# Kernel optimization log

Hardware: AMD Instinct MI355X
Metric: run time of the kernel (lower is better)

The kernel has to match this reference:

```python
import jax, jax.numpy as jnp
import numpy as np

N_NODES = 50000
N_EDGES = 800000
D = 64
STEPS = 10
NEG_SLOPE = 0.2


def setup_inputs() -> dict:
    key = jax.random.key(0)
    ks = jax.random.split(key, 9)
    x = jax.random.normal(ks[0], (N_NODES, D), dtype=jnp.float32)
    edge_index_l1 = jax.random.randint(ks[1], (2, N_EDGES), 0, N_NODES, dtype=jnp.int64 if jax.config.jax_enable_x64 else jnp.int32)
    edge_index_l2 = jax.random.randint(ks[2], (2, N_EDGES), 0, N_NODES, dtype=jnp.int64 if jax.config.jax_enable_x64 else jnp.int32)
    s = 1.0 / np.sqrt(D)
    W1 = jax.random.normal(ks[3], (D, D), dtype=jnp.float32) * s
    a1_src = jax.random.normal(ks[4], (D,), dtype=jnp.float32) * s
    a1_dst = jax.random.normal(ks[5], (D,), dtype=jnp.float32) * s
    W2 = jax.random.normal(ks[6], (D, D), dtype=jnp.float32) * s
    a2_src = jax.random.normal(ks[7], (D,), dtype=jnp.float32) * s
    a2_dst = jax.random.normal(ks[8], (D,), dtype=jnp.float32) * s
    return {
        "x": x,
        "edge_index_l1": edge_index_l1,
        "edge_index_l2": edge_index_l2,
        "W1": W1, "a1_src": a1_src, "a1_dst": a1_dst,
        "W2": W2, "a2_src": a2_src, "a2_dst": a2_dst,
    }


def _gat_layer(x, src, dst, W, a_src, a_dst):
    """Single-head GATConv: out_i = sum_{j->i} softmax_i(LeakyReLU(a_s.Wx_j + a_d.Wx_i)) * Wx_j."""
    h = x @ W                                            # [N, D]
    e = jax.nn.leaky_relu((h @ a_src)[src] + (h @ a_dst)[dst], NEG_SLOPE)  # [E]
    # numerically stable segment softmax over incoming edges of each dst node
    m = jax.ops.segment_max(e, dst, num_segments=N_NODES)
    m = jax.lax.stop_gradient(jnp.where(jnp.isfinite(m), m, 0.0))
    w = jnp.exp(e - m[dst])                              # [E]
    denom = jax.ops.segment_sum(w, dst, num_segments=N_NODES)
    att = w / (denom[dst] + 1e-16)                       # [E]
    return jax.ops.segment_sum(h[src] * att[:, None], dst, num_segments=N_NODES)


def _base_operator(xt, ei1, ei2, W1, a1_src, a1_dst, W2, a2_src, a2_dst):
    h = _gat_layer(xt, ei1[0], ei1[1], W1, a1_src, a1_dst)
    h = jax.nn.elu(h)
    return _gat_layer(h, ei2[0], ei2[1], W2, a2_src, a2_dst)


def reference(x, edge_index_l1, edge_index_l2, W1, a1_src, a1_dst, W2, a2_src, a2_dst):
    ts = jnp.linspace(0.0, 1.0, STEPS, dtype=x.dtype)    # [STEPS]
    h_step = ts[1] - ts[0]                               # trapezoid-like uniform weight

    def step(acc, t):
        out = _base_operator(x * t, edge_index_l1, edge_index_l2,
                             W1, a1_src, a1_dst, W2, a2_src, a2_dst)
        return acc + out, None

    result, _ = jax.lax.scan(step, jnp.zeros_like(x), ts)
    return result * h_step
```

## Files before the change

### kernel.cpp

```cpp
#include <hip/hip_runtime.h>
#include <hip/hip_bf16.h>

#define NN 50000
#define NE 800000
#define DD 64
#define NEG 0.2f

#define RFL(x) __builtin_amdgcn_readfirstlane(x)

__global__ void k_hist(const int* __restrict__ dst1, const int* __restrict__ dst2,
                       int* __restrict__ cnt1, int* __restrict__ cnt2) {
    int t = blockIdx.x * blockDim.x + threadIdx.x;
    if (t < NE / 4) {
        int4 d1 = ((const int4*)dst1)[t];
        int4 d2 = ((const int4*)dst2)[t];
        atomicAdd(&cnt1[d1.x], 1); atomicAdd(&cnt1[d1.y], 1);
        atomicAdd(&cnt1[d1.z], 1); atomicAdd(&cnt1[d1.w], 1);
        atomicAdd(&cnt2[d2.x], 1); atomicAdd(&cnt2[d2.y], 1);
        atomicAdd(&cnt2[d2.z], 1); atomicAdd(&cnt2[d2.w], 1);
    }
}

__global__ __launch_bounds__(1024) void k_scan(const int* __restrict__ cnt1, int* __restrict__ off1,
                                               const int* __restrict__ cnt2, int* __restrict__ off2) {
    const int* cnt = blockIdx.x ? cnt2 : cnt1;
    int* off = blockIdx.x ? off2 : off1;
    __shared__ int lds[1024];
    const int tid = threadIdx.x;
    const int CH = (NN + 1023) / 1024;
    const int base = tid * CH;
    int s = 0;
    for (int q = 0; q < CH; ++q) {
        int idx = base + q;
        if (idx < NN) s += cnt[idx];
    }
    lds[tid] = s;
    __syncthreads();
    for (int d = 1; d < 1024; d <<= 1) {
        int v = (tid >= d) ? lds[tid - d] : 0;
        __syncthreads();
        lds[tid] += v;
        __syncthreads();
    }
    int run = tid ? lds[tid - 1] : 0;
    for (int q = 0; q < CH; ++q) {
        int idx = base + q;
        if (idx < NN) { off[idx] = run; run += cnt[idx]; }
    }
    if (tid == 1023) off[NN] = lds[1023];
}

__global__ void k_scatter(const int* __restrict__ src1, const int* __restrict__ dst1,
                          const int* __restrict__ off1, int* __restrict__ fill1, int* __restrict__ csr1,
                          const int* __restrict__ src2, const int* __restrict__ dst2,
                          const int* __restrict__ off2, int* __restrict__ fill2, int* __restrict__ csr2) {
    int t = blockIdx.x * blockDim.x + threadIdx.x;
    if (t < NE / 4) {
        int4 s1 = ((const int4*)src1)[t];
        int4 d1 = ((const int4*)dst1)[t];
        int4 s2 = ((const int4*)src2)[t];
        int4 d2 = ((const int4*)dst2)[t];
        int pA = off1[d1.x] + atomicAdd(&fill1[d1.x], 1);
        int pB = off1[d1.y] + atomicAdd(&fill1[d1.y], 1);
        int pC = off1[d1.z] + atomicAdd(&fill1[d1.z], 1);
        int pD = off1[d1.w] + atomicAdd(&fill1[d1.w], 1);
        int qA = off2[d2.x] + atomicAdd(&fill2[d2.x], 1);
        int qB = off2[d2.y] + atomicAdd(&fill2[d2.y], 1);
        int qC = off2[d2.z] + atomicAdd(&fill2[d2.z], 1);
        int qD = off2[d2.w] + atomicAdd(&fill2[d2.w], 1);
        csr1[pA] = s1.x; csr1[pB] = s1.y; csr1[pC] = s1.z; csr1[pD] = s1.w;
        csr2[qA] = s2.x; csr2[qB] = s2.y; csr2[qC] = s2.z; csr2[qD] = s2.w;
    }
}

__global__ __launch_bounds__(256) void k_h1(
    const float* __restrict__ x, const float* __restrict__ W1,
    const float* __restrict__ a1s, const float* __restrict__ a1d,
    float* __restrict__ H1, float* __restrict__ al1s, float* __restrict__ al1d) {
    const int lane = threadIdx.x & 63;
    const int i = blockIdx.x * 4 + (threadIdx.x >> 6);
    const float xv = x[i * DD + lane];
    float h = 0.f;
#pragma unroll
    for (int j = 0; j < DD; ++j) h = fmaf(__shfl(xv, j), W1[j * DD + lane], h);
    H1[i * DD + lane] = h;
    float ps = h * a1s[lane], pd = h * a1d[lane];
#pragma unroll
    for (int o = 32; o; o >>= 1) { ps += __shfl_xor(ps, o); pd += __shfl_xor(pd, o); }
    if (lane == 0) { al1s[i] = ps; al1d[i] = pd; }
}

__global__ void k_a2t(const float* __restrict__ W2, const float* __restrict__ a2s,
                      const float* __restrict__ a2d, float* __restrict__ t2s,
                      float* __restrict__ t2d) {
    int j = threadIdx.x & 63;
    float ss = 0.f, sd = 0.f;
#pragma unroll
    for (int d = 0; d < DD; ++d) {
        float w = W2[j * DD + d];
        ss = fmaf(w, a2s[d], ss);
        sd = fmaf(w, a2d[d], sd);
    }
    t2s[j] = ss;
    t2d[j] = sd;
}

__global__ __launch_bounds__(256) void k_l1(
    const int* __restrict__ off, const int* __restrict__ csrc,
    const float* __restrict__ al1s, const float* __restrict__ al1d,
    const float* __restrict__ H1,
    const float* __restrict__ t2s, const float* __restrict__ t2d,
    uint4* __restrict__ H2a, _Float16* __restrict__ H2b,
    float* __restrict__ al2s8, float* __restrict__ al2s9, float* __restrict__ al2d) {
    __shared__ int2 lsr[4][64];
    const int lane = threadIdx.x & 63;
    const int wid = threadIdx.x >> 6;
    const int i = blockIdx.x * 4 + wid;
    const int p0 = RFL(off[i]);
    const int p1 = RFL(off[i + 1]);
    const float adv = al1d[i];
    float num[9], den[9];
#pragma unroll
    for (int k = 0; k < 9; ++k) { num[k] = 0.f; den[k] = 0.f; }

    for (int base = p0; base < p1; base += 64) {
        int m = p1 - base; if (m > 64) m = 64;
        int sv = 0; float rv = 0.f;
        if (lane < m) {
            sv = csrc[base + lane];
            float z = al1s[sv] + adv;
            float c = z > 0.f ? z : NEG * z;
            rv = __expf(c * (1.f / 9.f));
        }
        {
            float w = rv;
#pragma unroll
            for (int k = 0; k < 9; ++k) { den[k] += w; w *= rv; }
        }
        lsr[wid][lane] = make_int2(sv, __float_as_int(rv));
        asm volatile("s_waitcnt lgkmcnt(0)" ::: "memory");
        int j = 0;
        for (; j + 3 < m; j += 4) {
            int2 e0 = lsr[wid][j], e1 = lsr[wid][j + 1];
            int2 e2 = lsr[wid][j + 2], e3 = lsr[wid][j + 3];
            float h0 = H1[(size_t)e0.x * DD + lane];
            float h1v = H1[(size_t)e1.x * DD + lane];
            float h2v = H1[(size_t)e2.x * DD + lane];
            float h3v = H1[(size_t)e3.x * DD + lane];
            float r0 = __int_as_float(e0.y), r1 = __int_as_float(e1.y);
            float r2 = __int_as_float(e2.y), r3 = __int_as_float(e3.y);
            float w0 = r0, w1 = r1, w2 = r2, w3 = r3;
#pragma unroll
            for (int k = 0; k < 9; ++k) {
                num[k] = fmaf(w0, h0, num[k]);  w0 *= r0;
                num[k] = fmaf(w1, h1v, num[k]); w1 *= r1;
                num[k] = fmaf(w2, h2v, num[k]); w2 *= r2;
                num[k] = fmaf(w3, h3v, num[k]); w3 *= r3;
            }
        }
        for (; j < m; ++j) {
            int2 e0 = lsr[wid][j];
            float h0 = H1[(size_t)e0.x * DD + lane];
            float r0 = __int_as_float(e0.y);
            float w0 = r0;
#pragma unroll
            for (int k = 0; k < 9; ++k) { num[k] = fmaf(w0, h0, num[k]); w0 *= r0; }
        }
    }
#pragma unroll
    for (int k = 0; k < 9; ++k) {
#pragma unroll
        for (int o = 32; o; o >>= 1) den[k] += __shfl_xor(den[k], o);
    }

    const float tss = t2s[lane];
    const float tdd = t2d[lane];
    float hm[9];
#pragma unroll
    for (int k = 0; k < 9; ++k) {
        float t = (float)(k + 1) * (1.f / 9.f);
        float v = (den[k] > 0.f) ? (t * num[k] / den[k]) : 0.f;
        hm[k] = (v > 0.f) ? v : expm1f(v);
    }
#pragma unroll
    for (int k = 0; k < 9; ++k) {
        float ps = hm[k] * tss, pd = hm[k] * tdd;
#pragma unroll
        for (int o = 32; o; o >>= 1) { ps += __shfl_xor(ps, o); pd += __shfl_xor(pd, o); }
        if (lane == 0) {
            if (k < 8) al2s8[(size_t)i * 8 + k] = ps;
            else       al2s9[i] = ps;
            al2d[(size_t)i * 9 + k] = pd;
        }
    }
    union { _Float16 h[8]; uint4 u; } pk;
#pragma unroll
    for (int k = 0; k < 8; ++k) pk.h[k] = (_Float16)hm[k];
    H2a[(size_t)i * DD + lane] = pk.u;
    H2b[(size_t)i * DD + lane] = (_Float16)hm[8];
}

__global__ __launch_bounds__(256) void k_l2(
    const int* __restrict__ off, const int* __restrict__ csrc,
    const float* __restrict__ al2s8, const float* __restrict__ al2s9,
    const float* __restrict__ al2d,
    const uint4* __restrict__ H2a, const _Float16* __restrict__ H2b,
    const float* __restrict__ W2, float* __restrict__ out) {
    __shared__ float lw[4][64][12];
    const int lane = threadIdx.x & 63;
    const int wid = threadIdx.x >> 6;
    const int i = blockIdx.x * 4 + wid;
    const int p0 = RFL(off[i]);
    const int p1 = RFL(off[i + 1]);
    float adv[9];
#pragma unroll
    for (int k = 0; k < 9; ++k) adv[k] = al2d[(size_t)i * 9 + k];
    float num[9], den[9];
#pragma unroll
    for (int k = 0; k < 9; ++k) { num[k] = 0.f; den[k] = 0.f; }

    for (int base = p0; base < p1; base += 64) {
        int m = p1 - base; if (m > 64) m = 64;
        int sv = 0; float wv[9];
#pragma unroll
        for (int k = 0; k < 9; ++k) wv[k] = 0.f;
        if (lane < m) {
            sv = csrc[base + lane];
            const float4* pa = (const float4*)(al2s8 + (size_t)sv * 8);
            float4 A0 = pa[0], A1 = pa[1];
            float as[9] = {A0.x, A0.y, A0.z, A0.w, A1.x, A1.y, A1.z, A1.w, al2s9[sv]};
#pragma unroll
            for (int k = 0; k < 9; ++k) {
                float z = as[k] + adv[k];
                float lr = z > 0.f ? z : NEG * z;
                wv[k] = __expf(lr);
            }
        }
#pragma unroll
        for (int k = 0; k < 9; ++k) den[k] += wv[k];
        float* dst = &lw[wid][lane][0];
        *(float4*)dst       = make_float4(wv[0], wv[1], wv[2], wv[3]);
        *(float4*)(dst + 4) = make_float4(wv[4], wv[5], wv[6], wv[7]);
        dst[8] = wv[8];
        dst[9] = __int_as_float(sv);
        asm volatile("s_waitcnt lgkmcnt(0)" ::: "memory");
        int j = 0;
        for (; j + 1 < m; j += 2) {
            const float* s0 = &lw[wid][j][0];
            const float* s1 = &lw[wid][j + 1][0];
            int sj0 = __float_as_int(s0[9]);
            int sj1 = __float_as_int(s1[9]);
            union { uint4 v; _Float16 h[8]; } c0, c1;
            c0.v = H2a[(size_t)sj0 * DD + lane];
            c1.v = H2a[(size_t)sj1 * DD + lane];
            float h90 = (float)H2b[(size_t)sj0 * DD + lane];
            float h91 = (float)H2b[(size_t)sj1 * DD + lane];
            float4 wA0 = *(const float4*)s0, wB0 = *(const float4*)(s0 + 4);
            float4 wA1 = *(const float4*)s1, wB1 = *(const float4*)(s1 + 4);
            num[0] = fmaf(wA0.x, (float)c0.h[0], num[0]);
            num[1] = fmaf(wA0.y, (float)c0.h[1], num[1]);
            num[2] = fmaf(wA0.z, (float)c0.h[2], num[2]);
            num[3] = fmaf(wA0.w, (float)c0.h[3], num[3]);
            num[4] = fmaf(wB0.x, (float)c0.h[4], num[4]);
            num[5] = fmaf(wB0.y, (float)c0.h[5], num[5]);
            num[6] = fmaf(wB0.z, (float)c0.h[6], num[6]);
            num[7] = fmaf(wB0.w, (float)c0.h[7], num[7]);
            num[8] = fmaf(s0[8], h90, num[8]);
            num[0] = fmaf(wA1.x, (float)c1.h[0], num[0]);
            num[1] = fmaf(wA1.y, (float)c1.h[1], num[1]);
            num[2] = fmaf(wA1.z, (float)c1.h[2], num[2]);
            num[3] = fmaf(wA1.w, (float)c1.h[3], num[3]);
            num[4] = fmaf(wB1.x, (float)c1.h[4], num[4]);
            num[5] = fmaf(wB1.y, (float)c1.h[5], num[5]);
            num[6] = fmaf(wB1.z, (float)c1.h[6], num[6]);
            num[7] = fmaf(wB1.w, (float)c1.h[7], num[7]);
            num[8] = fmaf(s1[8], h91, num[8]);
        }
        if (j < m) {
            const float* s0 = &lw[wid][j][0];
            int sj0 = __float_as_int(s0[9]);
            union { uint4 v; _Float16 h[8]; } c0;
            c0.v = H2a[(size_t)sj0 * DD + lane];
            float h90 = (float)H2b[(size_t)sj0 * DD + lane];
            float4 wA0 = *(const float4*)s0, wB0 = *(const float4*)(s0 + 4);
            num[0] = fmaf(wA0.x, (float)c0.h[0], num[0]);
            num[1] = fmaf(wA0.y, (float)c0.h[1], num[1]);
            num[2] = fmaf(wA0.z, (float)c0.h[2], num[2]);
            num[3] = fmaf(wA0.w, (float)c0.h[3], num[3]);
            num[4] = fmaf(wB0.x, (float)c0.h[4], num[4]);
            num[5] = fmaf(wB0.y, (float)c0.h[5], num[5]);
            num[6] = fmaf(wB0.z, (float)c0.h[6], num[6]);
            num[7] = fmaf(wB0.w, (float)c0.h[7], num[7]);
            num[8] = fmaf(s0[8], h90, num[8]);
        }
    }
#pragma unroll
    for (int k = 0; k < 9; ++k) {
#pragma unroll
        for (int o = 32; o; o >>= 1) den[k] += __shfl_xor(den[k], o);
    }
    float vsum = 0.f;
#pragma unroll
    for (int k = 0; k < 9; ++k) vsum += (den[k] > 0.f) ? (num[k] / den[k]) : 0.f;
    float h2 = 0.f;
#pragma unroll 8
    for (int j = 0; j < DD; ++j) h2 = fmaf(__shfl(vsum, j), W2[j * DD + lane], h2);
    out[(size_t)i * DD + lane] = h2 * (1.f / 9.f);
}

extern "C" void kernel_launch(void* const* d_in, const int* in_sizes, int n_in,
                              void* d_out, int out_size, void* d_ws, size_t ws_size,
                              hipStream_t stream) {
    const float* x   = (const float*)d_in[0];
    const int*   ei1 = (const int*)d_in[1];
    const int*   ei2 = (const int*)d_in[2];
    const float* W1  = (const float*)d_in[3];
    const float* a1s = (const float*)d_in[4];
    const float* a1d = (const float*)d_in[5];
    const float* W2  = (const float*)d_in[6];
    const float* a2s = (const float*)d_in[7];
    const float* a2d = (const float*)d_in[8];
    float* out = (float*)d_out;

    const int* src1 = ei1;
    const int* dst1 = ei1 + NE;
    const int* src2 = ei2;
    const int* dst2 = ei2 + NE;

    uint4* H2a   = (uint4*)d_ws;
    float* H1    = (float*)d_ws + (size_t)NN * 256;
    float* al1s  = H1 + (size_t)NN * DD;
    float* al1d  = al1s + NN;
    float* al2s8 = al1d + NN;
    float* al2s9 = al2s8 + (size_t)NN * 8;
    float* al2d  = al2s9 + NN;
    _Float16* H2b = (_Float16*)(al2d + (size_t)NN * 9);
    int* off1 = (int*)((float*)H2b + (size_t)NN * DD / 2);
    int* off2 = off1 + (NN + 1);
    int* cnt1 = off2 + (NN + 1);
    int* cnt2 = cnt1 + NN;
    int* csr1 = cnt2 + NN;
    int* csr2 = csr1 + NE;
    float* t2s = (float*)(csr2 + NE);
    float* t2d = t2s + DD;

    const int EB = 256;
    const int EG4 = (NE / 4 + EB - 1) / EB;
    const int NB = NN / 4;

    hipMemsetAsync(cnt1, 0, 2 * NN * sizeof(int), stream);
    k_hist<<<EG4, EB, 0, stream>>>(dst1, dst2, cnt1, cnt2);
    k_scan<<<2, 1024, 0, stream>>>(cnt1, off1, cnt2, off2);
    hipMemsetAsync(cnt1, 0, 2 * NN * sizeof(int), stream);
    k_scatter<<<EG4, EB, 0, stream>>>(src1, dst1, off1, cnt1, csr1,
                                      src2, dst2, off2, cnt2, csr2);
    k_h1<<<NB, 256, 0, stream>>>(x, W1, a1s, a1d, H1, al1s, al1d);
    k_a2t<<<1, 64, 0, stream>>>(W2, a2s, a2d, t2s, t2d);

    k_l1<<<NB, 256, 0, stream>>>(off1, csr1, al1s, al1d, H1,
                                 t2s, t2d, H2a, H2b, al2s8, al2s9, al2d);
    k_l2<<<NB, 256, 0, stream>>>(off2, csr2, al2s8, al2s9, al2d, H2a, H2b, W2, out);
}
```

Measured before the change: 558.5 us.

## Reuse histogram atomic ranks for CSR placement, store H1 and CSR indices compactly

The histogram pass now records each edge's atomic return value as its rank, so the scatter pass places edges without a second round of atomics or a second memset. CSR source indices are stored as 16-bit values, since node ids fit below 65536. Layer-1 features H1 are stored in fp16 to halve the bytes gathered per edge in the layer-1 aggregation. This trades extra rank buffers and reduced H1 precision for less atomic traffic and less gather bandwidth.

Measured after the change: 473.9 us. -15.1%, faster.

```diff
diff --git a/kernel.cpp b/kernel.cpp
--- a/kernel.cpp
+++ b/kernel.cpp
@@ -7,17 +7,22 @@
 #define NEG 0.2f
 
 #define RFL(x) __builtin_amdgcn_readfirstlane(x)
+typedef unsigned short u16;
 
 __global__ void k_hist(const int* __restrict__ dst1, const int* __restrict__ dst2,
-                       int* __restrict__ cnt1, int* __restrict__ cnt2) {
+                       int* __restrict__ cnt1, int* __restrict__ cnt2,
+                       int* __restrict__ rank1, int* __restrict__ rank2) {
     int t = blockIdx.x * blockDim.x + threadIdx.x;
     if (t < NE / 4) {
         int4 d1 = ((const int4*)dst1)[t];
         int4 d2 = ((const int4*)dst2)[t];
-        atomicAdd(&cnt1[d1.x], 1); atomicAdd(&cnt1[d1.y], 1);
-        atomicAdd(&cnt1[d1.z], 1); atomicAdd(&cnt1[d1.w], 1);
-        atomicAdd(&cnt2[d2.x], 1); atomicAdd(&cnt2[d2.y], 1);
-        atomicAdd(&cnt2[d2.z], 1); atomicAdd(&cnt2[d2.w], 1);
+        int4 r1, r2;
+        r1.x = atomicAdd(&cnt1[d1.x], 1); r1.y = atomicAdd(&cnt1[d1.y], 1);
+        r1.z = atomicAdd(&cnt1[d1.z], 1); r1.w = atomicAdd(&cnt1[d1.w], 1);
+        r2.x = atomicAdd(&cnt2[d2.x], 1); r2.y = atomicAdd(&cnt2[d2.y], 1);
+        r2.z = atomicAdd(&cnt2[d2.z], 1); r2.w = atomicAdd(&cnt2[d2.w], 1);
+        ((int4*)rank1)[t] = r1;
+        ((int4*)rank2)[t] = r2;
     }
 }
 
@@ -50,40 +55,42 @@
     if (tid == 1023) off[NN] = lds[1023];
 }
 
-__global__ void k_scatter(const int* __restrict__ src1, const int* __restrict__ dst1,
-                          const int* __restrict__ off1, int* __restrict__ fill1, int* __restrict__ csr1,
-                          const int* __restrict__ src2, const int* __restrict__ dst2,
-                          const int* __restrict__ off2, int* __restrict__ fill2, int* __restrict__ csr2) {
+__global__ void k_place(const int* __restrict__ src1, const int* __restrict__ dst1,
+                        const int* __restrict__ off1, const int* __restrict__ rank1,
+                        u16* __restrict__ csr1,
+                        const int* __restrict__ src2, const int* __restrict__ dst2,
+                        const int* __restrict__ off2, const int* __restrict__ rank2,
+                        u16* __restrict__ csr2) {
     int t = blockIdx.x * blockDim.x + threadIdx.x;
     if (t < NE / 4) {
         int4 s1 = ((const int4*)src1)[t];
         int4 d1 = ((const int4*)dst1)[t];
+        int4 r1 = ((const int4*)rank1)[t];
         int4 s2 = ((const int4*)src2)[t];
         int4 d2 = ((const int4*)dst2)[t];
-        int pA = off1[d1.x] + atomicAdd(&fill1[d1.x], 1);
-        int pB = off1[d1.y] + atomicAdd(&fill1[d1.y], 1);
-        int pC = off1[d1.z] + atomicAdd(&fill1[d1.z], 1);
-        int pD = off1[d1.w] + atomicAdd(&fill1[d1.w], 1);
-        int qA = off2[d2.x] + atomicAdd(&fill2[d2.x], 1);
-        int qB = off2[d2.y] + atomicAdd(&fill2[d2.y], 1);
-        int qC = off2[d2.z] + atomicAdd(&fill2[d2.z], 1);
-        int qD = off2[d2.w] + atomicAdd(&fill2[d2.w], 1);
-        csr1[pA] = s1.x; csr1[pB] = s1.y; csr1[pC] = s1.z; csr1[pD] = s1.w;
-        csr2[qA] = s2.x; csr2[qB] = s2.y; csr2[qC] = s2.z; csr2[qD] = s2.w;
+        int4 r2 = ((const int4*)rank2)[t];
+        csr1[off1[d1.x] + r1.x] = (u16)s1.x;
+        csr1[off1[d1.y] + r1.y] = (u16)s1.y;
+        csr1[off1[d1.z] + r1.z] = (u16)s1.z;
+        csr1[off1[d1.w] + r1.w] = (u16)s1.w;
+        csr2[off2[d2.x] + r2.x] = (u16)s2.x;
+        csr2[off2[d2.y] + r2.y] = (u16)s2.y;
+        csr2[off2[d2.z] + r2.z] = (u16)s2.z;
+        csr2[off2[d2.w] + r2.w] = (u16)s2.w;
     }
 }
 
 __global__ __launch_bounds__(256) void k_h1(
     const float* __restrict__ x, const float* __restrict__ W1,
     const float* __restrict__ a1s, const float* __restrict__ a1d,
-    float* __restrict__ H1, float* __restrict__ al1s, float* __restrict__ al1d) {
+    _Float16* __restrict__ H1h, float* __restrict__ al1s, float* __restrict__ al1d) {
     const int lane = threadIdx.x & 63;
     const int i = blockIdx.x * 4 + (threadIdx.x >> 6);
     const float xv = x[i * DD + lane];
     float h = 0.f;
 #pragma unroll
     for (int j = 0; j < DD; ++j) h = fmaf(__shfl(xv, j), W1[j * DD + lane], h);
-    H1[i * DD + lane] = h;
+    H1h[(size_t)i * DD + lane] = (_Float16)h;
     float ps = h * a1s[lane], pd = h * a1d[lane];
 #pragma unroll
     for (int o = 32; o; o >>= 1) { ps += __shfl_xor(ps, o); pd += __shfl_xor(pd, o); }
@@ -106,9 +113,9 @@
 }
 
 __global__ __launch_bounds__(256) void k_l1(
-    const int* __restrict__ off, const int* __restrict__ csrc,
+    const int* __restrict__ off, const u16* __restrict__ csrc,
     const float* __restrict__ al1s, const float* __restrict__ al1d,
-    const float* __restrict__ H1,
+    const _Float16* __restrict__ H1h,
     const float* __restrict__ t2s, const float* __restrict__ t2d,
     uint4* __restrict__ H2a, _Float16* __restrict__ H2b,
     float* __restrict__ al2s8, float* __restrict__ al2s9, float* __restrict__ al2d) {
@@ -143,10 +150,10 @@
         for (; j + 3 < m; j += 4) {
             int2 e0 = lsr[wid][j], e1 = lsr[wid][j + 1];
             int2 e2 = lsr[wid][j + 2], e3 = lsr[wid][j + 3];
-            float h0 = H1[(size_t)e0.x * DD + lane];
-            float h1v = H1[(size_t)e1.x * DD + lane];
-            float h2v = H1[(size_t)e2.x * DD + lane];
-            float h3v = H1[(size_t)e3.x * DD + lane];
+            float h0 = (float)H1h[(size_t)e0.x * DD + lane];
+            float h1v = (float)H1h[(size_t)e1.x * DD + lane];
+            float h2v = (float)H1h[(size_t)e2.x * DD + lane];
+            float h3v = (float)H1h[(size_t)e3.x * DD + lane];
             float r0 = __int_as_float(e0.y), r1 = __int_as_float(e1.y);
             float r2 = __int_as_float(e2.y), r3 = __int_as_float(e3.y);
             float w0 = r0, w1 = r1, w2 = r2, w3 = r3;
@@ -160,7 +167,7 @@
         }
         for (; j < m; ++j) {
             int2 e0 = lsr[wid][j];
-            float h0 = H1[(size_t)e0.x * DD + lane];
+            float h0 = (float)H1h[(size_t)e0.x * DD + lane];
             float r0 = __int_as_float(e0.y);
             float w0 = r0;
 #pragma unroll
@@ -201,7 +208,7 @@
 }
 
 __global__ __launch_bounds__(256) void k_l2(
-    const int* __restrict__ off, const int* __restrict__ csrc,
+    const int* __restrict__ off, const u16* __restrict__ csrc,
     const float* __restrict__ al2s8, const float* __restrict__ al2s9,
     const float* __restrict__ al2d,
     const uint4* __restrict__ H2a, const _Float16* __restrict__ H2b,
@@ -327,37 +334,38 @@
     const int* src2 = ei2;
     const int* dst2 = ei2 + NE;
 
-    uint4* H2a   = (uint4*)d_ws;
-    float* H1    = (float*)d_ws + (size_t)NN * 256;
-    float* al1s  = H1 + (size_t)NN * DD;
-    float* al1d  = al1s + NN;
-    float* al2s8 = al1d + NN;
-    float* al2s9 = al2s8 + (size_t)NN * 8;
-    float* al2d  = al2s9 + NN;
+    uint4* H2a    = (uint4*)d_ws;
+    _Float16* H1h = (_Float16*)((float*)d_ws + (size_t)NN * 256);
+    float* al1s   = (float*)H1h + (size_t)NN * DD / 2;
+    float* al1d   = al1s + NN;
+    float* al2s8  = al1d + NN;
+    float* al2s9  = al2s8 + (size_t)NN * 8;
+    float* al2d   = al2s9 + NN;
     _Float16* H2b = (_Float16*)(al2d + (size_t)NN * 9);
-    int* off1 = (int*)((float*)H2b + (size_t)NN * DD / 2);
+    int* rank1 = (int*)((float*)H2b + (size_t)NN * DD / 2);
+    int* rank2 = rank1 + NE;
+    u16* csr1  = (u16*)(rank2 + NE);
+    u16* csr2  = csr1 + NE;
+    float* t2s = (float*)(csr2 + NE);
+    float* t2d = t2s + DD;
+    int* off1 = (int*)(t2d + DD);
     int* off2 = off1 + (NN + 1);
     int* cnt1 = off2 + (NN + 1);
     int* cnt2 = cnt1 + NN;
-    int* csr1 = cnt2 + NN;
-    int* csr2 = csr1 + NE;
-    float* t2s = (float*)(csr2 + NE);
-    float* t2d = t2s + DD;
 
     const int EB = 256;
     const int EG4 = (NE / 4 + EB - 1) / EB;
     const int NB = NN / 4;
 
     hipMemsetAsync(cnt1, 0, 2 * NN * sizeof(int), stream);
-    k_hist<<<EG4, EB, 0, stream>>>(dst1, dst2, cnt1, cnt2);
+    k_hist<<<EG4, EB, 0, stream>>>(dst1, dst2, cnt1, cnt2, rank1, rank2);
     k_scan<<<2, 1024, 0, stream>>>(cnt1, off1, cnt2, off2);
-    hipMemsetAsync(cnt1, 0, 2 * NN * sizeof(int), stream);
-    k_scatter<<<EG4, EB, 0, stream>>>(src1, dst1, off1, cnt1, csr1,
-                                      src2, dst2, off2, cnt2, csr2);
-    k_h1<<<NB, 256, 0, stream>>>(x, W1, a1s, a1d, H1, al1s, al1d);
+    k_place<<<EG4, EB, 0, stream>>>(src1, dst1, off1, rank1, csr1,
+                                    src2, dst2, off2, rank2, csr2);
+    k_h1<<<NB, 256, 0, stream>>>(x, W1, a1s, a1d, H1h, al1s, al1d);
     k_a2t<<<1, 64, 0, stream>>>(W2, a2s, a2d, t2s, t2d);
 
-    k_l1<<<NB, 256, 0, stream>>>(off1, csr1, al1s, al1d, H1,
+    k_l1<<<NB, 256, 0, stream>>>(off1, csr1, al1s, al1d, H1h,
                                  t2s, t2d, H2a, H2b, al2s8, al2s9, al2d);
     k_l2<<<NB, 256, 0, stream>>>(off2, csr2, al2s8, al2s9, al2d, H2a, H2b, W2, out);
 }
```
